# Kernel optimization log

Measured on AMD Instinct MI355X. Metric: run time of the kernel, lower is better.

## Reference

```python
import jax, jax.numpy as jnp
import numpy as np

IH, IW = 256, 704
FH, FW = 32, 88
D_MIN, D_MAX, D_RES = 1.0, 60.0, 0.5
D = int(np.ceil((D_MAX - D_MIN) / D_RES))  # 118 depth bins
C_IN, HID, C_OUT = 256, 64, 80
N_R, N_THETA = 128, 256
BN_EPS = 1e-5


def _edges():
    # non-uniform polar grid: angular bins uniform, radial bins grow with r
    ang = np.linspace(-np.pi / 2, np.pi / 2, N_THETA + 1).astype(np.float32)
    t = np.linspace(0.0, 1.0, N_R + 1)
    rad = (D_MIN + (t ** 1.5) * (D_MAX - D_MIN)).astype(np.float32)
    return jnp.asarray(ang), jnp.asarray(rad)


def _frustum():
    # [D, fH, fW, 3] of (u, v, depth) samples in image space
    ds = np.arange(D_MIN, D_MAX, D_RES, dtype=np.float32)
    xs = np.linspace(0, IW - 1, FW, dtype=np.float32)
    ys = np.linspace(0, IH - 1, FH, dtype=np.float32)
    d = np.broadcast_to(ds[:, None, None], (D, FH, FW))
    x = np.broadcast_to(xs[None, None, :], (D, FH, FW))
    y = np.broadcast_to(ys[None, :, None], (D, FH, FW))
    return jnp.asarray(np.stack([x, y, d], axis=-1))


def _bn(x, g, b, m, v):
    # inference-mode BatchNorm2d over channel axis 1; x: [BN, C, H, W]
    inv = g / jnp.sqrt(v + BN_EPS)
    return x * inv[None, :, None, None] + (b - m * inv)[None, :, None, None]


def setup_inputs() -> dict:
    key = jax.random.key(0)
    ks = jax.random.split(key, 8)
    B, N = 2, 1
    x = jax.random.normal(ks[0], (B, N, C_IN, FH, FW), dtype=jnp.float32)
    # camera->lidar axis permutation: x_l = z_c, y_l = -x_c, z_l = -y_c
    R = jnp.asarray([[0.0, 0.0, 1.0], [-1.0, 0.0, 0.0], [0.0, -1.0, 0.0]], dtype=jnp.float32)
    camera2lidar_rots = jnp.broadcast_to(R, (B, N, 3, 3))
    camera2lidar_trans = jnp.zeros((B, N, 3), dtype=jnp.float32)
    K = jnp.asarray([[380.0, 0.0, IW / 2.0], [0.0, 380.0, IH / 2.0], [0.0, 0.0, 1.0]], dtype=jnp.float32)
    intrins = jnp.broadcast_to(K, (B, N, 3, 3))
    s = 0.02
    params = dict(
        w1=jax.random.normal(ks[1], (HID, C_IN), dtype=jnp.float32) * s,
        b1=jnp.zeros((HID,), dtype=jnp.float32),
        g1=jnp.ones((HID,), dtype=jnp.float32),
        be1=jnp.zeros((HID,), dtype=jnp.float32),
        m1=jax.random.normal(ks[2], (HID,), dtype=jnp.float32) * s,
        v1=jnp.abs(jax.random.normal(ks[3], (HID,), dtype=jnp.float32)) + 0.5,
        w2=jax.random.normal(ks[4], (D + C_OUT, HID), dtype=jnp.float32) * s,
        b2=jnp.zeros((D + C_OUT,), dtype=jnp.float32),
        g2=jnp.ones((D + C_OUT,), dtype=jnp.float32),
        be2=jnp.zeros((D + C_OUT,), dtype=jnp.float32),
        m2=jax.random.normal(ks[5], (D + C_OUT,), dtype=jnp.float32) * s,
        v2=jnp.abs(jax.random.normal(ks[6], (D + C_OUT,), dtype=jnp.float32)) + 0.5,
    )
    return dict(x=x, camera2lidar_rots=camera2lidar_rots,
                camera2lidar_trans=camera2lidar_trans, intrins=intrins, **params)


def reference(x, camera2lidar_rots, camera2lidar_trans, intrins,
              w1, b1, g1, be1, m1, v1, w2, b2, g2, be2, m2, v2):
    B, N = x.shape[0], x.shape[1]
    # --- LIFT: DepthNet (two 1x1 convs + BN) -> depth dist x features outer product ---
    xf = x.reshape(B * N, C_IN, FH, FW)
    h = jnp.einsum('bchw,oc->bohw', xf, w1) + b1[None, :, None, None]
    h = jax.nn.relu(_bn(h, g1, be1, m1, v1))
    h = jnp.einsum('bchw,oc->bohw', h, w2) + b2[None, :, None, None]
    h = _bn(h, g2, be2, m2, v2)
    depth = jax.nn.softmax(h[:, :D], axis=1)            # [BN, D, fH, fW]
    feat = h[:, D:D + C_OUT]                            # [BN, C, fH, fW]
    lifted = depth[:, None, :, :, :] * feat[:, :, None, :, :]   # [BN, C, D, fH, fW]
    lifted = lifted.reshape(B, N, C_OUT, D, FH, FW).transpose(0, 1, 3, 4, 5, 2)  # [B,N,D,fH,fW,C]

    # --- geometry: unproject frustum to lidar frame ---
    fr = _frustum()                                      # [D, fH, fW, 3]
    u, v_, d = fr[..., 0], fr[..., 1], fr[..., 2]
    fx = intrins[..., 0, 0][:, :, None, None, None]
    fy = intrins[..., 1, 1][:, :, None, None, None]
    cx = intrins[..., 0, 2][:, :, None, None, None]
    cy = intrins[..., 1, 2][:, :, None, None, None]
    pc = jnp.stack([(u - cx) * d / fx, (v_ - cy) * d / fy,
                    jnp.broadcast_to(d, (B, N, D, FH, FW))], axis=-1)  # [B,N,D,fH,fW,3]
    pts = jnp.einsum('bnij,bndhwj->bndhwi', camera2lidar_rots, pc)
    pts = pts + camera2lidar_trans[:, :, None, None, None, :]

    # --- SPLAT: scatter-sum into non-uniform polar BEV grid ---
    ang_e, rad_e = _edges()
    xl, yl = pts[..., 0], pts[..., 1]
    r = jnp.sqrt(xl * xl + yl * yl)
    th = jnp.arctan2(yl, xl)
    r_idx = jnp.searchsorted(rad_e, r, side='right') - 1   # non-uniform bins -> bucketize
    t_idx = jnp.searchsorted(ang_e, th, side='right') - 1
    valid = (r_idx >= 0) & (r_idx < N_R) & (t_idx >= 0) & (t_idx < N_THETA)
    b_idx = jnp.arange(B)[:, None, None, None, None]
    trash = B * N_R * N_THETA  # dummy segment for out-of-grid points
    seg = jnp.where(valid, (b_idx * N_R + r_idx) * N_THETA + t_idx, trash).reshape(-1)
    bev = jax.ops.segment_sum(lifted.reshape(-1, C_OUT), seg, num_segments=trash + 1)[:-1]
    bev = bev.reshape(B, N_R, N_THETA, C_OUT).transpose(0, 3, 1, 2)  # [B, C, n_r, n_theta]
    return bev
```

## Files before the change

kernel.cpp:

```cpp
#include <hip/hip_runtime.h>
#include <hip/hip_bf16.h>
#include <hip/hip_cooperative_groups.h>
#include <math.h>

namespace cg = cooperative_groups;

#define FH 32
#define FW 88
#define DD 118
#define C_IN 256
#define HID 64
#define C_OUT 80
#define NPIX 5632
#define PIX_PER_B 2816
#define N_R 128
#define N_THETA 256
#define NCOL 176
#define NBIN 32768
#define ECAP 12
#define PSTRIDE 9440

#define FRONT_MLP  352
#define FRONT_BINS 82
#define FRONT_ZERO 320
#define FRONT_TOTAL (FRONT_MLP + FRONT_BINS + FRONT_ZERO)

typedef __attribute__((ext_vector_type(8))) short short8;
typedef __attribute__((ext_vector_type(4))) float f32x4;

__device__ inline float bf2f(unsigned short h) {
  return __uint_as_float((unsigned)h << 16);
}
__device__ inline unsigned short f2bf(float f) {
  unsigned u = __float_as_uint(f);
  unsigned r = (u + 0x7fffu + ((u >> 16) & 1u)) >> 16;
  return (unsigned short)r;
}
__device__ inline bool detect_bf16(const void* intr) {
  float f = __uint_as_float(*(const unsigned*)intr);
  return !(f > 300.0f && f < 500.0f);
}
__device__ inline float ldf(const void* p, int i, bool isb) {
  return isb ? bf2f(((const unsigned short*)p)[i]) : ((const float*)p)[i];
}

__device__ inline void load_geom(int tid, float* radEL, float* angEL, float* camsL,
                                 const void* rots, const void* trans, const void* intr,
                                 bool isb) {
  if (tid < 129) {
    double t = (double)tid * (1.0 / 128.0);
    radEL[tid] = (float)(1.0 + pow(t, 1.5) * 59.0);
  }
  for (int i = tid; i < 257; i += 256) {
    double step = M_PI / 256.0;
    double vv = (i == 256) ? (M_PI / 2.0) : ((double)i * step + (-M_PI / 2.0));
    angEL[i] = (float)vv;
  }
  if (tid < 18) camsL[tid] = ldf(rots, tid, isb);
  if (tid < 6)  camsL[20 + tid] = ldf(trans, tid, isb);
  if (tid >= 6 && tid < 24) camsL[28 + (tid - 6)] = ldf(intr, tid - 6, isb);
}

__device__ inline int computeBin(int w, int h, int d,
                                 const float* camsF, int b,
                                 const float* radE, const float* angE) {
  float fx = camsF[28 + b * 9 + 0], cx = camsF[28 + b * 9 + 2];
  float fy = camsF[28 + b * 9 + 4], cy = camsF[28 + b * 9 + 5];
  float R00 = camsF[b * 9 + 0], R01 = camsF[b * 9 + 1], R02 = camsF[b * 9 + 2];
  float R10 = camsF[b * 9 + 3], R11 = camsF[b * 9 + 4], R12 = camsF[b * 9 + 5];
  float Tx = camsF[20 + b * 3 + 0], Ty = camsF[20 + b * 3 + 1];
  float u  = (w == FW - 1) ? 703.0f : (float)((double)w * (703.0 / 87.0));
  float vv = (h == FH - 1) ? 255.0f : (float)((double)h * (255.0 / 31.0));
  float dd = 1.0f + 0.5f * (float)d;
  float px = __fdiv_rn(__fmul_rn(__fsub_rn(u, cx), dd), fx);
  float py = __fdiv_rn(__fmul_rn(__fsub_rn(vv, cy), dd), fy);
  float xl = __fadd_rn(__fadd_rn(__fadd_rn(__fmul_rn(R00, px), __fmul_rn(R01, py)),
                                 __fmul_rn(R02, dd)), Tx);
  float yl = __fadd_rn(__fadd_rn(__fadd_rn(__fmul_rn(R10, px), __fmul_rn(R11, py)),
                                 __fmul_rn(R12, dd)), Ty);
  float r = __fsqrt_rn(__fadd_rn(__fmul_rn(xl, xl), __fmul_rn(yl, yl)));
  float th = (float)atan2((double)yl, (double)xl);
  int lo = 0, hi = 129;
  while (lo < hi) { int mid = (lo + hi) >> 1; if (radE[mid] <= r) lo = mid + 1; else hi = mid; }
  int ri = lo - 1;
  lo = 0; hi = 257;
  while (lo < hi) { int mid = (lo + hi) >> 1; if (angE[mid] <= th) lo = mid + 1; else hi = mid; }
  int ti = lo - 1;
  bool valid = (ri >= 0) && (ri < N_R) && (ti >= 0) && (ti < N_THETA);
  return valid ? (ri * N_THETA + ti) : -1;
}


__device__ __forceinline__ void dev_mlp(
    int pix0, int tid, float* shbuf, float* h1L,
    float* inv1L, float* b1fL, float* inv2L, float* b2fL,
    const void* __restrict__ xraw,
    const void* __restrict__ w1r, const void* __restrict__ b1r,
    const void* __restrict__ g1r, const void* __restrict__ be1r,
    const void* __restrict__ m1r, const void* __restrict__ v1r,
    const void* __restrict__ w2r, const void* __restrict__ b2r,
    const void* __restrict__ g2r, const void* __restrict__ be2r,
    const void* __restrict__ m2r, const void* __restrict__ v2r,
    float* __restrict__ depthW, float* __restrict__ featW, bool isb) {
  unsigned short* xsU = (unsigned short*)shbuf;
  float* h2s = shbuf;
  float* smaxL = shbuf + 3200;
  float* ssumL = shbuf + 3456;
  if (tid < 64) {
    float iv = ldf(g1r, tid, isb) / sqrtf(ldf(v1r, tid, isb) + 1e-5f);
    inv1L[tid] = iv;
    b1fL[tid] = ldf(b1r, tid, isb) * iv + (ldf(be1r, tid, isb) - ldf(m1r, tid, isb) * iv);
  }
  if (tid < 198) {
    float iv = ldf(g2r, tid, isb) / sqrtf(ldf(v2r, tid, isb) + 1e-5f);
    inv2L[tid] = iv;
    b2fL[tid] = ldf(b2r, tid, isb) * iv + (ldf(be2r, tid, isb) - ldf(m2r, tid, isb) * iv);
  }
  int b = pix0 / PIX_PER_B;
  int ploc0 = pix0 - b * PIX_PER_B;
  size_t xbase = (size_t)b * C_IN * PIX_PER_B + ploc0;
  const unsigned short* xh = (const unsigned short*)xraw;
  const float* xf = (const float*)xraw;
  {
    int p = tid & 15, crow = tid >> 4;
    for (int it = 0; it < 16; it++) {
      int c = it * 16 + crow;
      size_t gi = xbase + (size_t)c * PIX_PER_B + p;
      xsU[p * 264 + c] = isb ? xh[gi] : f2bf(xf[gi]);
    }
  }
  int lane = tid & 63, wv = tid >> 6;
  int nloc = lane & 15, quad = lane >> 4;
  int orow = wv * 16 + nloc;
  short8 afr[8];
  const unsigned short* w1h = (const unsigned short*)w1r;
  const float* w1f32 = (const float*)w1r;
  if (isb) {
#pragma unroll
    for (int s = 0; s < 8; s++)
      afr[s] = *(const short8*)(w1h + orow * 256 + s * 32 + quad * 8);
  } else {
#pragma unroll
    for (int s = 0; s < 8; s++) {
      short8 a;
#pragma unroll
      for (int j = 0; j < 8; j++)
        a[j] = (short)f2bf(w1f32[orow * 256 + s * 32 + quad * 8 + j]);
      afr[s] = a;
    }
  }
  __syncthreads();
  f32x4 acc = {0.f, 0.f, 0.f, 0.f};
#pragma unroll
  for (int s = 0; s < 8; s++) {
    short8 bfr = *(const short8*)(xsU + nloc * 264 + s * 32 + quad * 8);
    acc = __builtin_amdgcn_mfma_f32_16x16x32_bf16(afr[s], bfr, acc, 0, 0, 0);
  }
#pragma unroll
  for (int r = 0; r < 4; r++) {
    int mm = wv * 16 + quad * 4 + r;
    float hv = fmaxf(fmaf(acc[r], inv1L[mm], b1fL[mm]), 0.f);
    h1L[nloc * 68 + mm] = hv;
  }
  __syncthreads();
  int p = tid & 15, g = tid >> 4;
  float h1v[64];
  const float4* hp = (const float4*)(h1L + p * 68);
#pragma unroll
  for (int k4 = 0; k4 < 16; k4++) {
    float4 hv = hp[k4];
    h1v[4 * k4 + 0] = hv.x; h1v[4 * k4 + 1] = hv.y;
    h1v[4 * k4 + 2] = hv.z; h1v[4 * k4 + 3] = hv.w;
  }
  for (int j = 0; j < 13; j++) {
    int o = g * 13 + j;
    if (o < 198) {
      float iv = inv2L[o];
      float q0 = 0.f, q1 = 0.f, q2 = 0.f, q3 = 0.f;
      if (isb) {
        const ushort4* wr = (const ushort4*)w2r;
#pragma unroll
        for (int k4 = 0; k4 < 16; k4 += 4) {
          ushort4 u0 = wr[o * 16 + k4 + 0];
          ushort4 u1 = wr[o * 16 + k4 + 1];
          ushort4 u2 = wr[o * 16 + k4 + 2];
          ushort4 u3 = wr[o * 16 + k4 + 3];
          q0 = fmaf(bf2f(u0.x) * iv, h1v[4 * k4 + 0], q0);
          q0 = fmaf(bf2f(u0.y) * iv, h1v[4 * k4 + 1], q0);
          q0 = fmaf(bf2f(u0.z) * iv, h1v[4 * k4 + 2], q0);
          q0 = fmaf(bf2f(u0.w) * iv, h1v[4 * k4 + 3], q0);
          q1 = fmaf(bf2f(u1.x) * iv, h1v[4 * k4 + 4], q1);
          q1 = fmaf(bf2f(u1.y) * iv, h1v[4 * k4 + 5], q1);
          q1 = fmaf(bf2f(u1.z) * iv, h1v[4 * k4 + 6], q1);
          q1 = fmaf(bf2f(u1.w) * iv, h1v[4 * k4 + 7], q1);
          q2 = fmaf(bf2f(u2.x) * iv, h1v[4 * k4 + 8], q2);
          q2 = fmaf(bf2f(u2.y) * iv, h1v[4 * k4 + 9], q2);
          q2 = fmaf(bf2f(u2.z) * iv, h1v[4 * k4 + 10], q2);
          q2 = fmaf(bf2f(u2.w) * iv, h1v[4 * k4 + 11], q2);
          q3 = fmaf(bf2f(u3.x) * iv, h1v[4 * k4 + 12], q3);
          q3 = fmaf(bf2f(u3.y) * iv, h1v[4 * k4 + 13], q3);
          q3 = fmaf(bf2f(u3.z) * iv, h1v[4 * k4 + 14], q3);
          q3 = fmaf(bf2f(u3.w) * iv, h1v[4 * k4 + 15], q3);
        }
      } else {
        const float4* wr = (const float4*)w2r;
#pragma unroll
        for (int k4 = 0; k4 < 16; k4 += 4) {
          float4 w0 = wr[o * 16 + k4 + 0];
          float4 w1v = wr[o * 16 + k4 + 1];
          float4 w2v = wr[o * 16 + k4 + 2];
          float4 w3v = wr[o * 16 + k4 + 3];
          q0 = fmaf(w0.x * iv, h1v[4 * k4 + 0], q0);
          q0 = fmaf(w0.y * iv, h1v[4 * k4 + 1], q0);
          q0 = fmaf(w0.z * iv, h1v[4 * k4 + 2], q0);
          q0 = fmaf(w0.w * iv, h1v[4 * k4 + 3], q0);
          q1 = fmaf(w1v.x * iv, h1v[4 * k4 + 4], q1);
          q1 = fmaf(w1v.y * iv, h1v[4 * k4 + 5], q1);
          q1 = fmaf(w1v.z * iv, h1v[4 * k4 + 6], q1);
          q1 = fmaf(w1v.w * iv, h1v[4 * k4 + 7], q1);
          q2 = fmaf(w2v.x * iv, h1v[4 * k4 + 8], q2);
          q2 = fmaf(w2v.y * iv, h1v[4 * k4 + 9], q2);
          q2 = fmaf(w2v.z * iv, h1v[4 * k4 + 10], q2);
          q2 = fmaf(w2v.w * iv, h1v[4 * k4 + 11], q2);
          q3 = fmaf(w3v.x * iv, h1v[4 * k4 + 12], q3);
          q3 = fmaf(w3v.y * iv, h1v[4 * k4 + 13], q3);
          q3 = fmaf(w3v.z * iv, h1v[4 * k4 + 14], q3);
          q3 = fmaf(w3v.w * iv, h1v[4 * k4 + 15], q3);
        }
      }
      h2s[o * 16 + p] = b2fL[o] + ((q0 + q1) + (q2 + q3));
    }
  }
  __syncthreads();
  int r0 = g * 8, r1 = min(118, r0 + 8);
  float lm = -INFINITY;
  for (int o = r0; o < r1; o++) lm = fmaxf(lm, h2s[o * 16 + p]);
  smaxL[g * 16 + p] = lm;
  __syncthreads();
  float m = smaxL[p];
#pragma unroll
  for (int gg = 1; gg < 16; gg++) m = fmaxf(m, smaxL[gg * 16 + p]);
  float ls = 0.f;
  for (int o = r0; o < r1; o++) ls += expf(h2s[o * 16 + p] - m);
  ssumL[g * 16 + p] = ls;
  __syncthreads();
  float tot = 0.f;
#pragma unroll
  for (int gg = 0; gg < 16; gg++) tot += ssumL[gg * 16 + p];
  int pix = pix0 + p;
  for (int o = r0; o < r1; o++)
    depthW[(size_t)pix * DD + o] = expf(h2s[o * 16 + p] - m) / tot;
  int f0 = g * 5;
  for (int f = f0; f < f0 + 5; f++)
    featW[(size_t)pix * C_OUT + f] = h2s[(118 + f) * 16 + p];
}

__device__ __forceinline__ void dev_bins(
    int blk_rel, int tid, float* radEL, float* angEL, float* camsL,
    const void* rots, const void* trans, const void* intr, bool isb,
    int* __restrict__ cnt, unsigned* __restrict__ ent, int* __restrict__ flag) {
  int t = blk_rel * 256 + tid;
  load_geom(tid, radEL, angEL, camsL, rots, trans, intr, isb);
  __syncthreads();
  if (t < NCOL * DD) {
    int col = t / DD, d = t - col * DD;
    int b = col / FW, w = col - b * FW;
    float R01 = camsL[b * 9 + 1], R11 = camsL[b * 9 + 4];
    if (!(R01 == 0.0f && R11 == 0.0f)) atomicOr(flag, 1);
    int bin = computeBin(w, 0, d, camsL, b, radEL, angEL);
    if (bin >= 0) {
      int slot = atomicAdd(&cnt[b * NBIN + bin], 1);
      if (slot < ECAP) ent[(size_t)(b * NBIN + bin) * ECAP + slot] = ((unsigned)col << 8) | (unsigned)d;
      else atomicOr(flag, 1);
    }
  }
}

__device__ __forceinline__ void dev_pcol(
    int col, int tid, float* depthL, float* featL,
    const float* __restrict__ depthW, const float* __restrict__ featW,
    float* __restrict__ P) {
  int b = col / FW, w = col - b * FW;
  size_t colPix = (size_t)b * PIX_PER_B + w;
  for (int i = tid; i < FH * DD; i += 256) {
    int h = i / DD, d = i - h * DD;
    depthL[h * 120 + d] = depthW[(colPix + (size_t)h * FW) * DD + d];
  }
  for (int i = tid; i < FH * C_OUT; i += 256) {
    int h = i / C_OUT, c = i - h * C_OUT;
    featL[i] = featW[(colPix + (size_t)h * FW) * C_OUT + c];
  }
  __syncthreads();
  const float4* featL4 = (const float4*)featL;
  const float4* depthL4 = (const float4*)depthL;
  float4* P4 = (float4*)(P + (size_t)col * PSTRIDE);
  for (int t = tid; t < 30 * 20; t += 256) {
    int dq = t / 20, c4 = t - dq * 20;
    float4 a0 = make_float4(0.f, 0.f, 0.f, 0.f);
    float4 a1 = make_float4(0.f, 0.f, 0.f, 0.f);
    float4 a2 = make_float4(0.f, 0.f, 0.f, 0.f);
    float4 a3 = make_float4(0.f, 0.f, 0.f, 0.f);
#pragma unroll
    for (int h = 0; h < FH; h++) {
      float4 wd = depthL4[h * 30 + dq];
      float4 f = featL4[h * 20 + c4];
      a0.x = fmaf(wd.x, f.x, a0.x); a0.y = fmaf(wd.x, f.y, a0.y);
      a0.z = fmaf(wd.x, f.z, a0.z); a0.w = fmaf(wd.x, f.w, a0.w);
      a1.x = fmaf(wd.y, f.x, a1.x); a1.y = fmaf(wd.y, f.y, a1.y);
      a1.z = fmaf(wd.y, f.z, a1.z); a1.w = fmaf(wd.y, f.w, a1.w);
      a2.x = fmaf(wd.z, f.x, a2.x); a2.y = fmaf(wd.z, f.y, a2.y);
      a2.z = fmaf(wd.z, f.z, a2.z); a2.w = fmaf(wd.z, f.w, a2.w);
      a3.x = fmaf(wd.w, f.x, a3.x); a3.y = fmaf(wd.w, f.y, a3.y);
      a3.z = fmaf(wd.w, f.z, a3.z); a3.w = fmaf(wd.w, f.w, a3.w);
    }
    int d0 = dq * 4;
    P4[(d0 + 0) * 20 + c4] = a0;
    P4[(d0 + 1) * 20 + c4] = a1;
    if (d0 + 2 < DD) {
      P4[(d0 + 2) * 20 + c4] = a2;
      P4[(d0 + 3) * 20 + c4] = a3;
    }
  }
}

__device__ __forceinline__ void dev_scatter(
    int idx2, int tid, float* depthL, float* featL,
    float* radEL, float* angEL, float* camsL,
    const void* rots, const void* trans, const void* intr, bool isb,
    const float* __restrict__ depthW, const float* __restrict__ featW,
    float* __restrict__ bevAcc) {
  int col = idx2 >> 1, chalf = idx2 & 1;
  int b = col / FW, w = col - b * FW;
  load_geom(tid, radEL, angEL, camsL, rots, trans, intr, isb);
  size_t colPix = (size_t)b * PIX_PER_B + w;
  for (int i = tid; i < FH * DD; i += 256) {
    int h = i / DD, d = i - h * DD;
    depthL[d * 33 + h] = depthW[(colPix + (size_t)h * FW) * DD + d];
  }
  for (int i = tid; i < FH * C_OUT; i += 256) {
    int h = i / C_OUT, c = i - h * C_OUT;
    featL[i] = featW[(colPix + (size_t)h * FW) * C_OUT + c];
  }
  __syncthreads();
  const float4* featL4 = (const float4*)featL;
  for (int t = tid; t < DD * FH * 10; t += 256) {
    int d = t / 320, rem = t - d * 320;
    int h = rem / 10, c4 = chalf * 10 + (rem - (rem / 10) * 10);
    int bin = computeBin(w, h, d, camsL, b, radEL, angEL);
    if (bin < 0) continue;
    float wd = depthL[d * 33 + h];
    float4 f = featL4[h * 20 + c4];
    float* outb = bevAcc + (((size_t)(b * C_OUT + c4 * 4)) << 15) + bin;
    unsafeAtomicAdd(outb, wd * f.x);
    unsafeAtomicAdd(outb + (1u << 15), wd * f.y);
    unsafeAtomicAdd(outb + (2u << 15), wd * f.z);
    unsafeAtomicAdd(outb + (3u << 15), wd * f.w);
  }
}

__device__ __forceinline__ void dev_out_main(
    int vt, int tid, const float* __restrict__ P,
    const int* __restrict__ cnt, const unsigned* __restrict__ ent,
    void* __restrict__ out, bool isb) {
  int b = vt >> 7;
  int ri = vt & 127;
  int bin = ri * N_THETA + tid;
  int n = cnt[b * NBIN + bin];
  if (n > ECAP) n = ECAP;
  unsigned ee[ECAP];
  const unsigned* eb = ent + (size_t)(b * NBIN + bin) * ECAP;
  for (int i = 0; i < n; i++) ee[i] = eb[i];
  for (int i = 1; i < n; i++) {
    unsigned key = ee[i]; int j = i - 1;
    while (j >= 0 && ee[j] > key) { ee[j + 1] = ee[j]; j--; }
    ee[j + 1] = key;
  }
  int base[ECAP];
  for (int i = 0; i < n; i++)
    base[i] = (int)(((ee[i] >> 8) * PSTRIDE + (ee[i] & 255u) * C_OUT) >> 2);
  const float4* P4 = (const float4*)P;
  unsigned short* oh = (unsigned short*)out;
  float* of = (float*)out;
  size_t obase = (((size_t)(b * C_OUT)) << 15) + bin;
  for (int c4 = 0; c4 < 20; c4++) {
    float4 s = make_float4(0.f, 0.f, 0.f, 0.f);
    for (int i = 0; i < n; i++) {
      float4 v = P4[base[i] + c4];
      s.x += v.x; s.y += v.y; s.z += v.z; s.w += v.w;
    }
    size_t o0 = obase + ((size_t)(c4 * 4) << 15);
    if (isb) {
      oh[o0]              = f2bf(s.x);
      oh[o0 + (1u << 15)] = f2bf(s.y);
      oh[o0 + (2u << 15)] = f2bf(s.z);
      oh[o0 + (3u << 15)] = f2bf(s.w);
    } else {
      of[o0]              = s.x;
      of[o0 + (1u << 15)] = s.y;
      of[o0 + (2u << 15)] = s.z;
      of[o0 + (3u << 15)] = s.w;
    }
  }
}

__device__ __forceinline__ void dev_out_copy(
    int gtid, int gstride, const float* __restrict__ bevAcc,
    void* __restrict__ out, bool isb) {
  const float4* a4 = (const float4*)bevAcc;
  int n4 = (NBIN * 2 * C_OUT) / 4;
  if (isb) {
    ushort4* o4 = (ushort4*)out;
    for (int i = gtid; i < n4; i += gstride) {
      float4 v = a4[i];
      ushort4 o; o.x = f2bf(v.x); o.y = f2bf(v.y); o.z = f2bf(v.z); o.w = f2bf(v.w);
      o4[i] = o;
    }
  } else {
    float4* o4 = (float4*)out;
    for (int i = gtid; i < n4; i += gstride) o4[i] = a4[i];
  }
}

__global__ __launch_bounds__(256) void k_fused(
    const void* __restrict__ xraw,
    const void* __restrict__ rots, const void* __restrict__ trans,
    const void* __restrict__ intr,
    const void* __restrict__ w1r, const void* __restrict__ b1r,
    const void* __restrict__ g1r, const void* __restrict__ be1r,
    const void* __restrict__ m1r, const void* __restrict__ v1r,
    const void* __restrict__ w2r, const void* __restrict__ b2r,
    const void* __restrict__ g2r, const void* __restrict__ be2r,
    const void* __restrict__ m2r, const void* __restrict__ v2r,
    int* __restrict__ cnt, unsigned* __restrict__ ent, int* __restrict__ flag,
    float* __restrict__ depthW, float* __restrict__ featW,
    float* __restrict__ bevAcc, float* __restrict__ P, void* __restrict__ out) {
  __shared__ __align__(16) float SH[6464];
  __shared__ float inv1L[64], b1fL[64], inv2L[198], b2fL[198];
  __shared__ float radEL[129], angEL[257], camsL[46];
  cg::grid_group grid = cg::this_grid();
  int tid = threadIdx.x;
  int bid = blockIdx.x, nb = gridDim.x;
  bool isb = detect_bf16(intr);

  for (int vb = bid; vb < FRONT_MLP + FRONT_BINS; vb += nb) {
    if (vb < FRONT_MLP) {
      dev_mlp(vb * 16, tid, SH, SH + 3712, inv1L, b1fL, inv2L, b2fL,
              xraw, w1r, b1r, g1r, be1r, m1r, v1r,
              w2r, b2r, g2r, be2r, m2r, v2r, depthW, featW, isb);
    } else {
      dev_bins(vb - FRONT_MLP, tid, radEL, angEL, camsL,
               rots, trans, intr, isb, cnt, ent, flag);
    }
    __syncthreads();
  }
  grid.sync();

  int fl = *(volatile int*)flag;
  if (fl == 0) {
    for (int col = bid; col < NCOL; col += nb) {
      dev_pcol(col, tid, SH, SH + 3840, depthW, featW, P);
      __syncthreads();
    }
    grid.sync();
    for (int vt = bid; vt < 2 * N_R; vt += nb)
      dev_out_main(vt, tid, P, cnt, ent, out, isb);
  } else {
    float4 z = make_float4(0.f, 0.f, 0.f, 0.f);
    float4* bz = (float4*)bevAcc;
    int n4 = (NBIN * 2 * C_OUT) / 4;
    for (int i = bid * 256 + tid; i < n4; i += nb * 256) bz[i] = z;
    grid.sync();
    for (int vt = bid; vt < NCOL * 2; vt += nb) {
      dev_scatter(vt, tid, SH, SH + 3896, radEL, angEL, camsL,
                  rots, trans, intr, isb, depthW, featW, bevAcc);
      __syncthreads();
    }
    grid.sync();
    dev_out_copy(bid * 256 + tid, nb * 256, bevAcc, out, isb);
  }
}

__global__ __launch_bounds__(256) void k_front(
    const void* __restrict__ xraw,
    const void* __restrict__ rots, const void* __restrict__ trans,
    const void* __restrict__ intr,
    const void* __restrict__ w1r, const void* __restrict__ b1r,
    const void* __restrict__ g1r, const void* __restrict__ be1r,
    const void* __restrict__ m1r, const void* __restrict__ v1r,
    const void* __restrict__ w2r, const void* __restrict__ b2r,
    const void* __restrict__ g2r, const void* __restrict__ be2r,
    const void* __restrict__ m2r, const void* __restrict__ v2r,
    int* __restrict__ cnt, unsigned* __restrict__ ent, int* __restrict__ flag,
    float* __restrict__ depthW, float* __restrict__ featW,
    float* __restrict__ bevAcc) {
  __shared__ __align__(16) float shbuf[3712];
  __shared__ __align__(16) float h1L[16 * 68];
  __shared__ float inv1L[64], b1fL[64], inv2L[198], b2fL[198];
  __shared__ float radEL[129], angEL[257], camsL[46];
  int tid = threadIdx.x;
  bool isb = detect_bf16(intr);
  if (blockIdx.x >= FRONT_MLP + FRONT_BINS) {
    int zb = blockIdx.x - (FRONT_MLP + FRONT_BINS);
    float4 z = make_float4(0.f, 0.f, 0.f, 0.f);
    float4* bz = (float4*)bevAcc;
    int n4 = (NBIN * 2 * C_OUT) / 4;
    for (int i = zb * 256 + tid; i < n4; i += FRONT_ZERO * 256) bz[i] = z;
    return;
  }
  if (blockIdx.x >= FRONT_MLP) {
    dev_bins(blockIdx.x - FRONT_MLP, tid, radEL, angEL, camsL,
             rots, trans, intr, isb, cnt, ent, flag);
    return;
  }
  dev_mlp(blockIdx.x * 16, tid, shbuf, h1L, inv1L, b1fL, inv2L, b2fL,
          xraw, w1r, b1r, g1r, be1r, m1r, v1r,
          w2r, b2r, g2r, be2r, m2r, v2r, depthW, featW, isb);
}

__global__ __launch_bounds__(256) void k_back(const float* __restrict__ depthW,
                                              const float* __restrict__ featW,
                                              const int* __restrict__ flag,
                                              const void* __restrict__ rots,
                                              const void* __restrict__ trans,
                                              const void* __restrict__ intr,
                                              float* __restrict__ P,
                                              float* __restrict__ bevAcc) {
  __shared__ __align__(16) float depthL[DD * 33];
  __shared__ __align__(16) float featL[FH * C_OUT];
  __shared__ float radEL[129], angEL[257], camsL[46];
  __shared__ int flagS;
  int tid = threadIdx.x;
  if (tid == 0) flagS = *flag;
  __syncthreads();
  if (blockIdx.x < NCOL) {
    if (flagS != 0) return;
    dev_pcol(blockIdx.x, tid, depthL, featL, depthW, featW, P);
    return;
  }
  if (flagS == 0) return;
  bool isb = detect_bf16(intr);
  dev_scatter(blockIdx.x - NCOL, tid, depthL, featL, radEL, angEL, camsL,
              rots, trans, intr, isb, depthW, featW, bevAcc);
}

__global__ __launch_bounds__(256) void k_out(const float* __restrict__ P,
                                             const int* __restrict__ cnt,
                                             const unsigned* __restrict__ ent,
                                             const int* __restrict__ flag,
                                             const float* __restrict__ bevAcc,
                                             void* __restrict__ out,
                                             const void* __restrict__ intrRaw) {
  bool isb = detect_bf16(intrRaw);
  int tid = threadIdx.x;
  if (*flag != 0) {
    dev_out_copy(blockIdx.x * 256 + tid, 1024 * 256, bevAcc, out, isb);
    return;
  }
  if (blockIdx.x < 2 * N_R)
    dev_out_main(blockIdx.x, tid, P, cnt, ent, out, isb);
}

extern "C" void kernel_launch(void* const* d_in, const int* in_sizes, int n_in,
                              void* d_out, int out_size, void* d_ws, size_t ws_size,
                              hipStream_t stream) {
  const void* x     = d_in[0];
  const void* rots  = d_in[1];
  const void* trans = d_in[2];
  const void* intr  = d_in[3];
  const void* w1  = d_in[4];
  const void* b1  = d_in[5];
  const void* g1  = d_in[6];
  const void* be1 = d_in[7];
  const void* m1  = d_in[8];
  const void* v1  = d_in[9];
  const void* w2  = d_in[10];
  const void* b2  = d_in[11];
  const void* g2  = d_in[12];
  const void* be2 = d_in[13];
  const void* m2  = d_in[14];
  const void* v2  = d_in[15];

  float* ws = (float*)d_ws;
  float*    P      = ws + 0;
  int*      cnt    = (int*)(ws + 1661440);
  int*      flag   = (int*)(ws + 1726976);
  unsigned* ent    = (unsigned*)(ws + 1727040);
  float*    depthW = ws + 2513472;
  float*    featW  = ws + 3178048;
  float*    bevAcc = ws + 3628608;

  static int g_init = 0;
  static int g_safe = -1;
  static int g_want = 0;
  if (!g_init) {
    g_init = 1;
    int dev = 0;
    (void)hipGetDevice(&dev);
    int coop = 0, numCU = 0, maxb = 0;
    (void)hipDeviceGetAttribute(&coop, hipDeviceAttributeCooperativeLaunch, dev);
    (void)hipDeviceGetAttribute(&numCU, hipDeviceAttributeMultiprocessorCount, dev);
    hipError_t e = hipOccupancyMaxActiveBlocksPerMultiprocessor(&maxb, (const void*)k_fused, 256, 0);
    if (coop && numCU > 0) {
      int cap = (e == hipSuccess && maxb > 0) ? maxb : 1;
      long s = (long)cap * (long)numCU;
      g_safe = (int)(s > 512 ? 512 : s);
      int w = 2 * numCU; if (w > 512) w = 512;
      g_want = (w > g_safe) ? w : 0;
    } else {
      g_safe = -1;
    }
  }

  (void)hipMemsetAsync(cnt, 0, (size_t)(65536 + 64) * sizeof(int), stream);

  if (g_safe > 0) {
    void* ka[24] = { (void*)&x, (void*)&rots, (void*)&trans, (void*)&intr,
                     (void*)&w1, (void*)&b1, (void*)&g1, (void*)&be1,
                     (void*)&m1, (void*)&v1, (void*)&w2, (void*)&b2,
                     (void*)&g2, (void*)&be2, (void*)&m2, (void*)&v2,
                     (void*)&cnt, (void*)&ent, (void*)&flag,
                     (void*)&depthW, (void*)&featW, (void*)&bevAcc,
                     (void*)&P, (void*)&d_out };
    if (g_want > 0) {
      hipStreamCaptureStatus cs = hipStreamCaptureStatusNone;
      hipError_t qe = hipStreamIsCapturing(stream, &cs);
      if (qe == hipSuccess && cs == hipStreamCaptureStatusNone) {
        hipError_t e = hipLaunchCooperativeKernel((const void*)k_fused, dim3(g_want),
                                                  dim3(256), ka, 0u, stream);
        if (e == hipSuccess) { g_safe = g_want; g_want = 0; return; }
        (void)hipGetLastError();
        g_want = 0;
      }
    }
    hipError_t e = hipLaunchCooperativeKernel((const void*)k_fused, dim3(g_safe),
                                              dim3(256), ka, 0u, stream);
    if (e == hipSuccess) return;
    (void)hipGetLastError();
    g_safe = -1;
  }

  k_front<<<FRONT_TOTAL, 256, 0, stream>>>(x, rots, trans, intr,
                                           w1, b1, g1, be1, m1, v1,
                                           w2, b2, g2, be2, m2, v2,
                                           cnt, ent, flag, depthW, featW, bevAcc);
  k_back<<<NCOL * 3, 256, 0, stream>>>(depthW, featW, flag, rots, trans, intr, P, bevAcc);
  k_out<<<1024, 256, 0, stream>>>(P, cnt, ent, flag, bevAcc, d_out, intr);
}
```

Baseline: 146.4 us.

## Replace cooperative fused kernel with chain of specialized stream-ordered kernels

Removes the cooperative-launch persistent kernel that relied on grid-wide syncs, and splits the work into seven separate kernels (MLP, bins, pcol, zero, scatter, gather-out, copy) ordered on the stream. Each kernel checks the flag and exits early when its path is not taken. This avoids grid.sync overhead and the occupancy limits of a persistent grid, but adds extra launch latency and kernel boundaries, and removes overlap between the MLP and bin-building stages.

```diff
diff --git a/kernel.cpp b/kernel.cpp
--- a/kernel.cpp
+++ b/kernel.cpp
@@ -1,9 +1,6 @@
 #include <hip/hip_runtime.h>
 #include <hip/hip_bf16.h>
-#include <hip/hip_cooperative_groups.h>
 #include <math.h>
-
-namespace cg = cooperative_groups;
 
 #define FH 32
 #define FW 88
@@ -19,11 +16,6 @@
 #define NBIN 32768
 #define ECAP 12
 #define PSTRIDE 9440
-
-#define FRONT_MLP  352
-#define FRONT_BINS 82
-#define FRONT_ZERO 320
-#define FRONT_TOTAL (FRONT_MLP + FRONT_BINS + FRONT_ZERO)
 
 typedef __attribute__((ext_vector_type(8))) short short8;
 typedef __attribute__((ext_vector_type(4))) float f32x4;
@@ -421,143 +413,83 @@
   }
 }
 
-__global__ __launch_bounds__(256) void k_fused(
+
+__global__ __launch_bounds__(256) void k_mlp(
     const void* __restrict__ xraw,
-    const void* __restrict__ rots, const void* __restrict__ trans,
-    const void* __restrict__ intr,
     const void* __restrict__ w1r, const void* __restrict__ b1r,
     const void* __restrict__ g1r, const void* __restrict__ be1r,
     const void* __restrict__ m1r, const void* __restrict__ v1r,
     const void* __restrict__ w2r, const void* __restrict__ b2r,
     const void* __restrict__ g2r, const void* __restrict__ be2r,
     const void* __restrict__ m2r, const void* __restrict__ v2r,
-    int* __restrict__ cnt, unsigned* __restrict__ ent, int* __restrict__ flag,
-    float* __restrict__ depthW, float* __restrict__ featW,
-    float* __restrict__ bevAcc, float* __restrict__ P, void* __restrict__ out) {
-  __shared__ __align__(16) float SH[6464];
-  __shared__ float inv1L[64], b1fL[64], inv2L[198], b2fL[198];
-  __shared__ float radEL[129], angEL[257], camsL[46];
-  cg::grid_group grid = cg::this_grid();
-  int tid = threadIdx.x;
-  int bid = blockIdx.x, nb = gridDim.x;
-  bool isb = detect_bf16(intr);
-
-  for (int vb = bid; vb < FRONT_MLP + FRONT_BINS; vb += nb) {
-    if (vb < FRONT_MLP) {
-      dev_mlp(vb * 16, tid, SH, SH + 3712, inv1L, b1fL, inv2L, b2fL,
-              xraw, w1r, b1r, g1r, be1r, m1r, v1r,
-              w2r, b2r, g2r, be2r, m2r, v2r, depthW, featW, isb);
-    } else {
-      dev_bins(vb - FRONT_MLP, tid, radEL, angEL, camsL,
-               rots, trans, intr, isb, cnt, ent, flag);
-    }
-    __syncthreads();
-  }
-  grid.sync();
-
-  int fl = *(volatile int*)flag;
-  if (fl == 0) {
-    for (int col = bid; col < NCOL; col += nb) {
-      dev_pcol(col, tid, SH, SH + 3840, depthW, featW, P);
-      __syncthreads();
-    }
-    grid.sync();
-    for (int vt = bid; vt < 2 * N_R; vt += nb)
-      dev_out_main(vt, tid, P, cnt, ent, out, isb);
-  } else {
-    float4 z = make_float4(0.f, 0.f, 0.f, 0.f);
-    float4* bz = (float4*)bevAcc;
-    int n4 = (NBIN * 2 * C_OUT) / 4;
-    for (int i = bid * 256 + tid; i < n4; i += nb * 256) bz[i] = z;
-    grid.sync();
-    for (int vt = bid; vt < NCOL * 2; vt += nb) {
-      dev_scatter(vt, tid, SH, SH + 3896, radEL, angEL, camsL,
-                  rots, trans, intr, isb, depthW, featW, bevAcc);
-      __syncthreads();
-    }
-    grid.sync();
-    dev_out_copy(bid * 256 + tid, nb * 256, bevAcc, out, isb);
-  }
-}
-
-__global__ __launch_bounds__(256) void k_front(
-    const void* __restrict__ xraw,
-    const void* __restrict__ rots, const void* __restrict__ trans,
     const void* __restrict__ intr,
-    const void* __restrict__ w1r, const void* __restrict__ b1r,
-    const void* __restrict__ g1r, const void* __restrict__ be1r,
-    const void* __restrict__ m1r, const void* __restrict__ v1r,
-    const void* __restrict__ w2r, const void* __restrict__ b2r,
-    const void* __restrict__ g2r, const void* __restrict__ be2r,
-    const void* __restrict__ m2r, const void* __restrict__ v2r,
-    int* __restrict__ cnt, unsigned* __restrict__ ent, int* __restrict__ flag,
-    float* __restrict__ depthW, float* __restrict__ featW,
-    float* __restrict__ bevAcc) {
+    float* __restrict__ depthW, float* __restrict__ featW) {
   __shared__ __align__(16) float shbuf[3712];
   __shared__ __align__(16) float h1L[16 * 68];
   __shared__ float inv1L[64], b1fL[64], inv2L[198], b2fL[198];
-  __shared__ float radEL[129], angEL[257], camsL[46];
-  int tid = threadIdx.x;
   bool isb = detect_bf16(intr);
-  if (blockIdx.x >= FRONT_MLP + FRONT_BINS) {
-    int zb = blockIdx.x - (FRONT_MLP + FRONT_BINS);
-    float4 z = make_float4(0.f, 0.f, 0.f, 0.f);
-    float4* bz = (float4*)bevAcc;
-    int n4 = (NBIN * 2 * C_OUT) / 4;
-    for (int i = zb * 256 + tid; i < n4; i += FRONT_ZERO * 256) bz[i] = z;
-    return;
-  }
-  if (blockIdx.x >= FRONT_MLP) {
-    dev_bins(blockIdx.x - FRONT_MLP, tid, radEL, angEL, camsL,
-             rots, trans, intr, isb, cnt, ent, flag);
-    return;
-  }
-  dev_mlp(blockIdx.x * 16, tid, shbuf, h1L, inv1L, b1fL, inv2L, b2fL,
+  dev_mlp(blockIdx.x * 16, threadIdx.x, shbuf, h1L, inv1L, b1fL, inv2L, b2fL,
           xraw, w1r, b1r, g1r, be1r, m1r, v1r,
           w2r, b2r, g2r, be2r, m2r, v2r, depthW, featW, isb);
 }
 
-__global__ __launch_bounds__(256) void k_back(const float* __restrict__ depthW,
-                                              const float* __restrict__ featW,
-                                              const int* __restrict__ flag,
-                                              const void* __restrict__ rots,
-                                              const void* __restrict__ trans,
-                                              const void* __restrict__ intr,
-                                              float* __restrict__ P,
-                                              float* __restrict__ bevAcc) {
+__global__ __launch_bounds__(256) void k_bins(
+    const void* __restrict__ rots, const void* __restrict__ trans,
+    const void* __restrict__ intr,
+    int* __restrict__ cnt, unsigned* __restrict__ ent, int* __restrict__ flag) {
+  __shared__ float radEL[129], angEL[257], camsL[46];
+  bool isb = detect_bf16(intr);
+  dev_bins(blockIdx.x, threadIdx.x, radEL, angEL, camsL,
+           rots, trans, intr, isb, cnt, ent, flag);
+}
+
+__global__ __launch_bounds__(256) void k_pcol(
+    const float* __restrict__ depthW, const float* __restrict__ featW,
+    const int* __restrict__ flag, float* __restrict__ P) {
+  __shared__ __align__(16) float depthL[32 * 120];
+  __shared__ __align__(16) float featL[FH * C_OUT];
+  if (*flag != 0) return;
+  dev_pcol(blockIdx.x, threadIdx.x, depthL, featL, depthW, featW, P);
+}
+
+__global__ __launch_bounds__(256) void k_zerofb(
+    const int* __restrict__ flag, float* __restrict__ bevAcc) {
+  if (*flag == 0) return;
+  float4 z = make_float4(0.f, 0.f, 0.f, 0.f);
+  float4* bz = (float4*)bevAcc;
+  int n4 = (NBIN * 2 * C_OUT) / 4;
+  for (int i = blockIdx.x * 256 + threadIdx.x; i < n4; i += 320 * 256) bz[i] = z;
+}
+
+__global__ __launch_bounds__(256) void k_scatter(
+    const float* __restrict__ depthW, const float* __restrict__ featW,
+    const int* __restrict__ flag,
+    const void* __restrict__ rots, const void* __restrict__ trans,
+    const void* __restrict__ intr, float* __restrict__ bevAcc) {
   __shared__ __align__(16) float depthL[DD * 33];
   __shared__ __align__(16) float featL[FH * C_OUT];
   __shared__ float radEL[129], angEL[257], camsL[46];
-  __shared__ int flagS;
-  int tid = threadIdx.x;
-  if (tid == 0) flagS = *flag;
-  __syncthreads();
-  if (blockIdx.x < NCOL) {
-    if (flagS != 0) return;
-    dev_pcol(blockIdx.x, tid, depthL, featL, depthW, featW, P);
-    return;
-  }
-  if (flagS == 0) return;
+  if (*flag == 0) return;
   bool isb = detect_bf16(intr);
-  dev_scatter(blockIdx.x - NCOL, tid, depthL, featL, radEL, angEL, camsL,
+  dev_scatter(blockIdx.x, threadIdx.x, depthL, featL, radEL, angEL, camsL,
               rots, trans, intr, isb, depthW, featW, bevAcc);
 }
 
-__global__ __launch_bounds__(256) void k_out(const float* __restrict__ P,
-                                             const int* __restrict__ cnt,
-                                             const unsigned* __restrict__ ent,
-                                             const int* __restrict__ flag,
-                                             const float* __restrict__ bevAcc,
-                                             void* __restrict__ out,
-                                             const void* __restrict__ intrRaw) {
+__global__ __launch_bounds__(256) void k_outg(
+    const float* __restrict__ P, const int* __restrict__ cnt,
+    const unsigned* __restrict__ ent, const int* __restrict__ flag,
+    void* __restrict__ out, const void* __restrict__ intrRaw) {
+  if (*flag != 0) return;
   bool isb = detect_bf16(intrRaw);
-  int tid = threadIdx.x;
-  if (*flag != 0) {
-    dev_out_copy(blockIdx.x * 256 + tid, 1024 * 256, bevAcc, out, isb);
-    return;
-  }
-  if (blockIdx.x < 2 * N_R)
-    dev_out_main(blockIdx.x, tid, P, cnt, ent, out, isb);
+  dev_out_main(blockIdx.x, threadIdx.x, P, cnt, ent, out, isb);
+}
+
+__global__ __launch_bounds__(256) void k_copy(
+    const float* __restrict__ bevAcc, const int* __restrict__ flag,
+    void* __restrict__ out, const void* __restrict__ intrRaw) {
+  if (*flag == 0) return;
+  bool isb = detect_bf16(intrRaw);
+  dev_out_copy(blockIdx.x * 256 + threadIdx.x, 1024 * 256, bevAcc, out, isb);
 }
 
 extern "C" void kernel_launch(void* const* d_in, const int* in_sizes, int n_in,
@@ -589,60 +521,14 @@
   float*    featW  = ws + 3178048;
   float*    bevAcc = ws + 3628608;
 
-  static int g_init = 0;
-  static int g_safe = -1;
-  static int g_want = 0;
-  if (!g_init) {
-    g_init = 1;
-    int dev = 0;
-    (void)hipGetDevice(&dev);
-    int coop = 0, numCU = 0, maxb = 0;
-    (void)hipDeviceGetAttribute(&coop, hipDeviceAttributeCooperativeLaunch, dev);
-    (void)hipDeviceGetAttribute(&numCU, hipDeviceAttributeMultiprocessorCount, dev);
-    hipError_t e = hipOccupancyMaxActiveBlocksPerMultiprocessor(&maxb, (const void*)k_fused, 256, 0);
-    if (coop && numCU > 0) {
-      int cap = (e == hipSuccess && maxb > 0) ? maxb : 1;
-      long s = (long)cap * (long)numCU;
-      g_safe = (int)(s > 512 ? 512 : s);
-      int w = 2 * numCU; if (w > 512) w = 512;
-      g_want = (w > g_safe) ? w : 0;
-    } else {
-      g_safe = -1;
-    }
-  }
-
   (void)hipMemsetAsync(cnt, 0, (size_t)(65536 + 64) * sizeof(int), stream);
 
-  if (g_safe > 0) {
-    void* ka[24] = { (void*)&x, (void*)&rots, (void*)&trans, (void*)&intr,
-                     (void*)&w1, (void*)&b1, (void*)&g1, (void*)&be1,
-                     (void*)&m1, (void*)&v1, (void*)&w2, (void*)&b2,
-                     (void*)&g2, (void*)&be2, (void*)&m2, (void*)&v2,
-                     (void*)&cnt, (void*)&ent, (void*)&flag,
-                     (void*)&depthW, (void*)&featW, (void*)&bevAcc,
-                     (void*)&P, (void*)&d_out };
-    if (g_want > 0) {
-      hipStreamCaptureStatus cs = hipStreamCaptureStatusNone;
-      hipError_t qe = hipStreamIsCapturing(stream, &cs);
-      if (qe == hipSuccess && cs == hipStreamCaptureStatusNone) {
-        hipError_t e = hipLaunchCooperativeKernel((const void*)k_fused, dim3(g_want),
-                                                  dim3(256), ka, 0u, stream);
-        if (e == hipSuccess) { g_safe = g_want; g_want = 0; return; }
-        (void)hipGetLastError();
-        g_want = 0;
-      }
-    }
-    hipError_t e = hipLaunchCooperativeKernel((const void*)k_fused, dim3(g_safe),
-                                              dim3(256), ka, 0u, stream);
-    if (e == hipSuccess) return;
-    (void)hipGetLastError();
-    g_safe = -1;
-  }
-
-  k_front<<<FRONT_TOTAL, 256, 0, stream>>>(x, rots, trans, intr,
-                                           w1, b1, g1, be1, m1, v1,
-                                           w2, b2, g2, be2, m2, v2,
-                                           cnt, ent, flag, depthW, featW, bevAcc);
-  k_back<<<NCOL * 3, 256, 0, stream>>>(depthW, featW, flag, rots, trans, intr, P, bevAcc);
-  k_out<<<1024, 256, 0, stream>>>(P, cnt, ent, flag, bevAcc, d_out, intr);
-}
+  k_mlp<<<352, 256, 0, stream>>>(x, w1, b1, g1, be1, m1, v1,
+                                 w2, b2, g2, be2, m2, v2, intr, depthW, featW);
+  k_bins<<<82, 256, 0, stream>>>(rots, trans, intr, cnt, ent, flag);
+  k_pcol<<<NCOL, 256, 0, stream>>>(depthW, featW, flag, P);
+  k_zerofb<<<320, 256, 0, stream>>>(flag, bevAcc);
+  k_scatter<<<NCOL * 2, 256, 0, stream>>>(depthW, featW, flag, rots, trans, intr, bevAcc);
+  k_outg<<<2 * N_R, 256, 0, stream>>>(P, cnt, ent, flag, d_out, intr);
+  k_copy<<<1024, 256, 0, stream>>>(bevAcc, flag, d_out, intr);
+}
```

Measured after the change: 154.1 us. 1.05x slower.
